# Optimization experiments

Measured on AMD Instinct MI355X. Metric: run time of the kernel, lower is better.

The kernel has to match this reference:

```python
import jax, jax.numpy as jnp
import numpy as np

FEAT, NHID, NHALF, NCLS = 256, 512, 256, 2

def _xavier(key, shape):
    fan_in, fan_out = shape[0], shape[1]
    limit = np.sqrt(6.0 / (fan_in + fan_out))
    return jax.random.uniform(key, shape, jnp.float32, -limit, limit)

def setup_inputs() -> dict:
    key = jax.random.key(0)
    ks = jax.random.split(key, 10)
    B, N = 64, 1024
    x = jax.random.normal(ks[0], (B, N, FEAT), jnp.float32)
    adj = jax.random.uniform(ks[1], (B, N, N), jnp.float32)
    adj = adj / jnp.sum(adj, axis=-1, keepdims=True)  # row-normalized (mean aggregation)
    return {
        "x": x, "adj": adj,
        "W1": _xavier(ks[2], (2 * FEAT, NHID)), "b1": jnp.zeros((NHID,), jnp.float32),
        "W2": _xavier(ks[3], (2 * NHID, NHID)), "b2": jnp.zeros((NHID,), jnp.float32),
        "W3": _xavier(ks[4], (2 * NHID, NHALF)), "b3": jnp.zeros((NHALF,), jnp.float32),
        "W4": _xavier(ks[5], (2 * NHALF, NHALF)), "b4": jnp.zeros((NHALF,), jnp.float32),
        "Wc1": _xavier(ks[6], (NHALF, NHALF)), "bc1": jnp.zeros((NHALF,), jnp.float32),
        "alpha": jnp.full((NHALF,), 0.25, jnp.float32),  # PReLU per-channel slope
        "Wc2": _xavier(ks[7], (NHALF, NCLS)), "bc2": jnp.zeros((NCLS,), jnp.float32),
    }

def _gconv(x, adj, W, b):
    # MeanAggregator: bmm(adj, x); GraphConv: relu(cat([x, agg]) @ W + b)
    agg = jnp.einsum('bnm,bmd->bnd', adj, x)
    cat = jnp.concatenate([x, agg], axis=-1)
    return jax.nn.relu(jnp.einsum('bnd,df->bnf', cat, W) + b)

def reference(x, adj, W1, b1, W2, b2, W3, b3, W4, b4, Wc1, bc1, alpha, Wc2, bc2):
    h = _gconv(x, adj, W1, b1)
    h = _gconv(h, adj, W2, b2)
    h = _gconv(h, adj, W3, b3)
    h = _gconv(h, adj, W4, b4)
    h = h.reshape(-1, h.shape[-1])  # [B*N, nhid_half]
    h = h @ Wc1 + bc1
    h = jnp.where(h > 0, h, alpha * h)  # PReLU
    logits = h @ Wc2 + bc2
    return jax.nn.log_softmax(logits, axis=-1)
```

## Files before the change

### kernel.cpp

```cpp
#include <hip/hip_runtime.h>
#include <hip/hip_bf16.h>
#include <cmath>

typedef _Float16 f16;
typedef __attribute__((ext_vector_type(4))) _Float16 f16x4;
typedef __attribute__((ext_vector_type(8))) _Float16 f16x8;
typedef __attribute__((ext_vector_type(4))) float f32x4;

__device__ inline void gload_lds16(const f16* g, f16* l) {
  __builtin_amdgcn_global_load_lds(
      (const __attribute__((address_space(1))) unsigned int*)g,
      (__attribute__((address_space(3))) unsigned int*)l, 16, 0, 0);
}

__global__ __launch_bounds__(256) void cvt_f32_f16(const float* __restrict__ in,
                                                   f16* __restrict__ out, long n) {
  long stride = (long)gridDim.x * 256 * 8;
  for (long i = ((long)blockIdx.x * 256 + threadIdx.x) * 8; i < n; i += stride) {
    float4 a = *(const float4*)(in + i);
    float4 b = *(const float4*)(in + i + 4);
    f16x8 o;
    o[0] = (f16)a.x; o[1] = (f16)a.y; o[2] = (f16)a.z; o[3] = (f16)a.w;
    o[4] = (f16)b.x; o[5] = (f16)b.y; o[6] = (f16)b.z; o[7] = (f16)b.w;
    *(f16x8*)(out + i) = o;
  }
}

__global__ __launch_bounds__(256) void transpose_cvt(const float* __restrict__ in,
                                                     f16* __restrict__ out,
                                                     int R, int C, long sIn, long sOut) {
  in  += (long)blockIdx.z * sIn;
  out += (long)blockIdx.z * sOut;
  __shared__ f16 t[32][34];
  const int tx = threadIdx.x, ty = threadIdx.y;
  const int c0 = blockIdx.x * 32, r0 = blockIdx.y * 32;
  #pragma unroll
  for (int j = 0; j < 32; j += 8)
    t[ty + j][tx] = (f16)in[(long)(r0 + ty + j) * C + (c0 + tx)];
  __syncthreads();
  #pragma unroll
  for (int j = 0; j < 32; j += 8)
    out[(long)(c0 + ty + j) * R + (r0 + tx)] = t[tx][ty + j];
}

template <int ACT, bool DUAL, bool WRITE_T>
__global__ __launch_bounds__(256) void gemm_nt(
    const f16* __restrict__ A1, int lda1,
    const f16* __restrict__ B1, int ldb1, int K1,
    const f16* __restrict__ A2, int lda2,
    const f16* __restrict__ B2, int ldb2, int K2,
    const float* __restrict__ bias, const float* __restrict__ alpha,
    f16* __restrict__ C, int ldc, f16* __restrict__ CT,
    long sA, long sB, long sC) {
  __shared__ f16 As[128 * 32];
  __shared__ f16 Bs[128 * 32];
  const int tid = threadIdx.x;
  const int z = blockIdx.z;
  const f16* pA1 = A1 + (long)z * sA;
  const f16* pB1 = B1 + (long)z * sB;
  f16* pC = C + (long)z * sC;
  const int m0 = blockIdx.x * 128, n0 = blockIdx.y * 128;
  const int lane = tid & 63, wid = tid >> 6;
  const int wm = (wid >> 1) * 64, wn = (wid & 1) * 64;
  const int lrow = lane & 15, kg = lane >> 4;

  f32x4 acc[4][4] = {};

  const f16* Ap = pA1;
  const f16* Bp = pB1;
  int ldA = lda1, ldB = ldb1, K = K1;
  for (int phase = 0; phase < (DUAL ? 2 : 1); ++phase) {
    if (DUAL && phase == 1) { Ap = A2; Bp = B2; ldA = lda2; ldB = ldb2; K = K2; }
    for (int k0 = 0; k0 < K; k0 += 32) {
      const f16* baseA = Ap + (long)m0 * ldA + k0;
      const f16* baseB = Bp + (long)n0 * ldB + k0;
      f16* dA = As + (tid & 192) * 8;
      f16* dB = Bs + (tid & 192) * 8;
      gload_lds16(baseA + (tid >> 2) * ldA + (tid & 3) * 8, dA);
      gload_lds16(baseB + (tid >> 2) * ldB + (tid & 3) * 8, dB);
      {
        const int idx = 256 + tid;
        gload_lds16(baseA + (idx >> 2) * ldA + (idx & 3) * 8, dA + 2048);
        gload_lds16(baseB + (idx >> 2) * ldB + (idx & 3) * 8, dB + 2048);
      }
      __syncthreads();
      f16x8 af[4], bf[4];
      #pragma unroll
      for (int m = 0; m < 4; ++m)
        af[m] = *(const f16x8*)&As[(wm + m * 16 + lrow) * 32 + kg * 8];
      #pragma unroll
      for (int n = 0; n < 4; ++n)
        bf[n] = *(const f16x8*)&Bs[(wn + n * 16 + lrow) * 32 + kg * 8];
      #pragma unroll
      for (int m = 0; m < 4; ++m)
        #pragma unroll
        for (int n = 0; n < 4; ++n)
          acc[m][n] = __builtin_amdgcn_mfma_f32_16x16x32_f16(af[m], bf[n], acc[m][n], 0, 0, 0);
      __syncthreads();
    }
  }

  #pragma unroll
  for (int n = 0; n < 4; ++n) {
    const int gn = n0 + wn + n * 16 + lrow;
    const float bv = bias ? bias[gn] : 0.0f;
    const float av = (ACT == 2) ? alpha[gn] : 0.0f;
    #pragma unroll
    for (int m = 0; m < 4; ++m) {
      const int rg0 = m0 + wm + m * 16 + kg * 4;
      f16 tv[4];
      #pragma unroll
      for (int r = 0; r < 4; ++r) {
        float v = acc[m][n][r] + bv;
        if (ACT == 1) v = fmaxf(v, 0.0f);
        if (ACT == 2) v = (v > 0.0f) ? v : av * v;
        const f16 h = (f16)v;
        tv[r] = h;
        pC[(long)(rg0 + r) * ldc + gn] = h;
      }
      if (WRITE_T) {
        const int b = rg0 >> 10, node = rg0 & 1023;
        f16x4 pk;
        pk[0] = tv[0]; pk[1] = tv[1]; pk[2] = tv[2]; pk[3] = tv[3];
        *(f16x4*)&CT[((long)b * ldc + gn) * 1024 + node] = pk;
      }
    }
  }
}

__global__ __launch_bounds__(256) void logits_lsm(const f16* __restrict__ hc,
                                                  const float* __restrict__ Wc2,
                                                  const float* __restrict__ bc2,
                                                  float* __restrict__ out) {
  __shared__ float w[512];
  __shared__ float bb[2];
  const int t = threadIdx.x;
  w[t] = Wc2[t];
  w[t + 256] = Wc2[t + 256];
  if (t < 2) bb[t] = bc2[t];
  __syncthreads();
  const long row = (long)blockIdx.x * 256 + t;
  const f16* hr = hc + row * 256;
  float l0 = 0.f, l1 = 0.f;
  #pragma unroll 4
  for (int d0 = 0; d0 < 256; d0 += 8) {
    f16x8 v = *(const f16x8*)(hr + d0);
    #pragma unroll
    for (int j = 0; j < 8; ++j) {
      const float p = (float)v[j];
      l0 += p * w[(d0 + j) * 2];
      l1 += p * w[(d0 + j) * 2 + 1];
    }
  }
  l0 += bb[0];
  l1 += bb[1];
  const float mx = fmaxf(l0, l1);
  const float lse = mx + logf(expf(l0 - mx) + expf(l1 - mx));
  out[row * 2] = l0 - lse;
  out[row * 2 + 1] = l1 - lse;
}

extern "C" void kernel_launch(void* const* d_in, const int* in_sizes, int n_in,
                              void* d_out, int out_size, void* d_ws, size_t ws_size,
                              hipStream_t stream) {
  const float* x     = (const float*)d_in[0];
  const float* adj   = (const float*)d_in[1];
  const float* W1    = (const float*)d_in[2];
  const float* b1    = (const float*)d_in[3];
  const float* W2    = (const float*)d_in[4];
  const float* b2    = (const float*)d_in[5];
  const float* W3    = (const float*)d_in[6];
  const float* b3    = (const float*)d_in[7];
  const float* W4    = (const float*)d_in[8];
  const float* b4    = (const float*)d_in[9];
  const float* Wc1   = (const float*)d_in[10];
  const float* bc1   = (const float*)d_in[11];
  const float* alpha = (const float*)d_in[12];
  const float* Wc2   = (const float*)d_in[13];
  const float* bc2   = (const float*)d_in[14];
  float* out = (float*)d_out;

  char* ws = (char*)d_ws;
  f16* adjB = (f16*)(ws + 0L);
  f16* xN   = (f16*)(ws + 134217728L);
  f16* xT   = (f16*)(ws + 167772160L);
  f16* agg  = (f16*)(ws + 201326592L);
  f16* hAN  = (f16*)(ws + 268435456L);
  f16* hAT  = (f16*)(ws + 335544320L);
  f16* hBN  = (f16*)(ws + 402653184L);
  f16* hBT  = (f16*)(ws + 469762048L);
  f16* WT1  = (f16*)(ws + 536870912L);
  f16* WT2  = (f16*)(ws + 537395200L);
  f16* WT3  = (f16*)(ws + 538443776L);
  f16* WT4  = (f16*)(ws + 538968064L);
  f16* WTc1 = (f16*)(ws + 539230208L);
  if (ws_size < (size_t)539361280L) return;

  const dim3 tb(32, 8, 1);

  cvt_f32_f16<<<2048, 256, 0, stream>>>(adj, adjB, 64L * 1024 * 1024);
  cvt_f32_f16<<<1024, 256, 0, stream>>>(x, xN, 64L * 1024 * 256);
  transpose_cvt<<<dim3(8, 32, 64), tb, 0, stream>>>(x, xT, 1024, 256, 1024L * 256, 256L * 1024);
  transpose_cvt<<<dim3(16, 16, 1), tb, 0, stream>>>(W1, WT1, 512, 512, 0, 0);
  transpose_cvt<<<dim3(16, 32, 1), tb, 0, stream>>>(W2, WT2, 1024, 512, 0, 0);
  transpose_cvt<<<dim3(8, 32, 1), tb, 0, stream>>>(W3, WT3, 1024, 256, 0, 0);
  transpose_cvt<<<dim3(8, 16, 1), tb, 0, stream>>>(W4, WT4, 512, 256, 0, 0);
  transpose_cvt<<<dim3(8, 8, 1), tb, 0, stream>>>(Wc1, WTc1, 256, 256, 0, 0);

  gemm_nt<0, false, false><<<dim3(8, 2, 64), 256, 0, stream>>>(
      adjB, 1024, xT, 1024, 1024,
      nullptr, 0, nullptr, 0, 0,
      nullptr, nullptr, agg, 256, nullptr,
      1024L * 1024, 256L * 1024, 1024L * 256);
  gemm_nt<1, true, true><<<dim3(512, 4, 1), 256, 0, stream>>>(
      xN, 256, WT1, 512, 256,
      agg, 256, WT1 + 256, 512, 256,
      b1, nullptr, hAN, 512, hAT, 0, 0, 0);

  gemm_nt<0, false, false><<<dim3(8, 4, 64), 256, 0, stream>>>(
      adjB, 1024, hAT, 1024, 1024,
      nullptr, 0, nullptr, 0, 0,
      nullptr, nullptr, agg, 512, nullptr,
      1024L * 1024, 512L * 1024, 1024L * 512);
  gemm_nt<1, true, true><<<dim3(512, 4, 1), 256, 0, stream>>>(
      hAN, 512, WT2, 1024, 512,
      agg, 512, WT2 + 512, 1024, 512,
      b2, nullptr, hBN, 512, hBT, 0, 0, 0);

  gemm_nt<0, false, false><<<dim3(8, 4, 64), 256, 0, stream>>>(
      adjB, 1024, hBT, 1024, 1024,
      nullptr, 0, nullptr, 0, 0,
      nullptr, nullptr, agg, 512, nullptr,
      1024L * 1024, 512L * 1024, 1024L * 512);
  gemm_nt<1, true, true><<<dim3(512, 2, 1), 256, 0, stream>>>(
      hBN, 512, WT3, 1024, 512,
      agg, 512, WT3 + 512, 1024, 512,
      b3, nullptr, hAN, 256, hAT, 0, 0, 0);

  gemm_nt<0, false, false><<<dim3(8, 2, 64), 256, 0, stream>>>(
      adjB, 1024, hAT, 1024, 1024,
      nullptr, 0, nullptr, 0, 0,
      nullptr, nullptr, agg, 256, nullptr,
      1024L * 1024, 256L * 1024, 1024L * 256);
  gemm_nt<1, true, false><<<dim3(512, 2, 1), 256, 0, stream>>>(
      hAN, 256, WT4, 512, 256,
      agg, 256, WT4 + 256, 512, 256,
      b4, nullptr, hBN, 256, nullptr, 0, 0, 0);

  gemm_nt<2, false, false><<<dim3(512, 2, 1), 256, 0, stream>>>(
      hBN, 256, WTc1, 256, 256,
      nullptr, 0, nullptr, 0, 0,
      bc1, alpha, hAN, 256, nullptr, 0, 0, 0);

  logits_lsm<<<256, 256, 0, stream>>>(hAN, Wc2, bc2, out);
}
```

Before: 1.276 ms.

## Replace 128x128 GEMM with double-buffered 256x256 tile, swizzled LDS and split-K-step MFMA

The GEMM kernel moves from 128x128 tiles with BK=32 and a single LDS buffer to 256x256 tiles with BK=64 and 512 threads. Global-to-LDS loads are double-buffered and prefetched two steps ahead, with explicit vmcnt waits and barriers in place of full syncthreads. LDS columns are XOR-swizzled to avoid bank conflicts, and s_setprio is raised around the MFMA bursts. This should raise arithmetic intensity and hide load latency, at the cost of 128KB of LDS per block, higher register pressure and fewer blocks for the small batched GEMMs.

Measured after the change: 1.125 ms. -11.8%, faster.

```diff
diff --git a/kernel.cpp b/kernel.cpp
--- a/kernel.cpp
+++ b/kernel.cpp
@@ -44,70 +44,105 @@
 }
 
 template <int ACT, bool DUAL, bool WRITE_T>
-__global__ __launch_bounds__(256) void gemm_nt(
+__global__ __launch_bounds__(512, 2) void gemm256(
     const f16* __restrict__ A1, int lda1,
-    const f16* __restrict__ B1, int ldb1, int K1,
+    const f16* __restrict__ B1, int ldb1, int k1,
     const f16* __restrict__ A2, int lda2,
-    const f16* __restrict__ B2, int ldb2, int K2,
+    const f16* __restrict__ B2, int ldb2, int k2,
     const float* __restrict__ bias, const float* __restrict__ alpha,
     f16* __restrict__ C, int ldc, f16* __restrict__ CT,
     long sA, long sB, long sC) {
-  __shared__ f16 As[128 * 32];
-  __shared__ f16 Bs[128 * 32];
+  __shared__ f16 As[2][16384];
+  __shared__ f16 Bs[2][16384];
   const int tid = threadIdx.x;
   const int z = blockIdx.z;
-  const f16* pA1 = A1 + (long)z * sA;
-  const f16* pB1 = B1 + (long)z * sB;
+  const f16* a1 = A1 + (long)z * sA;
+  const f16* b1 = B1 + (long)z * sB;
   f16* pC = C + (long)z * sC;
-  const int m0 = blockIdx.x * 128, n0 = blockIdx.y * 128;
-  const int lane = tid & 63, wid = tid >> 6;
-  const int wm = (wid >> 1) * 64, wn = (wid & 1) * 64;
+  const int m0 = blockIdx.x * 256, n0 = blockIdx.y * 256;
+  const int lane = tid & 63, w = tid >> 6;
+  const int wr = w >> 2, wc = w & 3;
   const int lrow = lane & 15, kg = lane >> 4;
-
-  f32x4 acc[4][4] = {};
-
-  const f16* Ap = pA1;
-  const f16* Bp = pB1;
-  int ldA = lda1, ldB = ldb1, K = K1;
-  for (int phase = 0; phase < (DUAL ? 2 : 1); ++phase) {
-    if (DUAL && phase == 1) { Ap = A2; Bp = B2; ldA = lda2; ldB = ldb2; K = K2; }
-    for (int k0 = 0; k0 < K; k0 += 32) {
-      const f16* baseA = Ap + (long)m0 * ldA + k0;
-      const f16* baseB = Bp + (long)n0 * ldB + k0;
-      f16* dA = As + (tid & 192) * 8;
-      f16* dB = Bs + (tid & 192) * 8;
-      gload_lds16(baseA + (tid >> 2) * ldA + (tid & 3) * 8, dA);
-      gload_lds16(baseB + (tid >> 2) * ldB + (tid & 3) * 8, dB);
-      {
-        const int idx = 256 + tid;
-        gload_lds16(baseA + (idx >> 2) * ldA + (idx & 3) * 8, dA + 2048);
-        gload_lds16(baseB + (idx >> 2) * ldB + (idx & 3) * 8, dB + 2048);
-      }
-      __syncthreads();
-      f16x8 af[4], bf[4];
-      #pragma unroll
-      for (int m = 0; m < 4; ++m)
-        af[m] = *(const f16x8*)&As[(wm + m * 16 + lrow) * 32 + kg * 8];
+  const int NT1 = k1 >> 6;
+  const int NT = NT1 + (DUAL ? (k2 >> 6) : 0);
+
+  const int srow = tid >> 3;
+  const int cg = (tid & 7) ^ (srow & 7);
+  const int ldst = (tid & 448) * 8;
+
+  const int swz = lrow & 7;
+  const int ac0 = ((0 * 4 + kg) ^ swz) * 8;
+  const int ac1 = ((4 + kg) ^ swz) * 8;
+  const int arow = wr * 128 + lrow;
+  const int brow = wc * 64 + lrow;
+
+  f32x4 acc[8][4] = {};
+
+  auto stage = [&](int kt) {
+    const f16 *Ab, *Bb; int la, lb, kk;
+    if (!DUAL || kt < NT1) { Ab = a1; Bb = b1; la = lda1; lb = ldb1; kk = kt << 6; }
+    else { Ab = A2; Bb = B2; la = lda2; lb = ldb2; kk = (kt - NT1) << 6; }
+    const int bs = kt & 1;
+    #pragma unroll
+    for (int j = 0; j < 4; ++j)
+      gload_lds16(Ab + (long)(m0 + srow + j * 64) * la + kk + cg * 8,
+                  &As[bs][j * 4096 + ldst]);
+    #pragma unroll
+    for (int j = 0; j < 4; ++j)
+      gload_lds16(Bb + (long)(n0 + srow + j * 64) * lb + kk + cg * 8,
+                  &Bs[bs][j * 4096 + ldst]);
+  };
+
+  stage(0);
+  stage(1);
+  asm volatile("s_waitcnt vmcnt(8)\n\ts_barrier" ::: "memory");
+
+  for (int t = 0; t < NT; ++t) {
+    const int bs = t & 1;
+    f16x8 af[8], bf[4];
+    #pragma unroll
+    for (int m = 0; m < 8; ++m)
+      af[m] = *(const f16x8*)&As[bs][(arow + m * 16) * 64 + ac0];
+    #pragma unroll
+    for (int n = 0; n < 4; ++n)
+      bf[n] = *(const f16x8*)&Bs[bs][(brow + n * 16) * 64 + ac0];
+    __builtin_amdgcn_s_setprio(1);
+    #pragma unroll
+    for (int m = 0; m < 8; ++m)
       #pragma unroll
       for (int n = 0; n < 4; ++n)
-        bf[n] = *(const f16x8*)&Bs[(wn + n * 16 + lrow) * 32 + kg * 8];
+        acc[m][n] = __builtin_amdgcn_mfma_f32_16x16x32_f16(af[m], bf[n], acc[m][n], 0, 0, 0);
+    __builtin_amdgcn_s_setprio(0);
+    f16x8 ag[8], bg[4];
+    #pragma unroll
+    for (int m = 0; m < 8; ++m)
+      ag[m] = *(const f16x8*)&As[bs][(arow + m * 16) * 64 + ac1];
+    #pragma unroll
+    for (int n = 0; n < 4; ++n)
+      bg[n] = *(const f16x8*)&Bs[bs][(brow + n * 16) * 64 + ac1];
+    asm volatile("s_waitcnt lgkmcnt(0)\n\ts_barrier" ::: "memory");
+    if (t + 2 < NT) stage(t + 2);
+    __builtin_amdgcn_s_setprio(1);
+    #pragma unroll
+    for (int m = 0; m < 8; ++m)
       #pragma unroll
-      for (int m = 0; m < 4; ++m)
-        #pragma unroll
-        for (int n = 0; n < 4; ++n)
-          acc[m][n] = __builtin_amdgcn_mfma_f32_16x16x32_f16(af[m], bf[n], acc[m][n], 0, 0, 0);
-      __syncthreads();
-    }
+      for (int n = 0; n < 4; ++n)
+        acc[m][n] = __builtin_amdgcn_mfma_f32_16x16x32_f16(ag[m], bg[n], acc[m][n], 0, 0, 0);
+    __builtin_amdgcn_s_setprio(0);
+    if (t + 2 < NT)
+      asm volatile("s_waitcnt vmcnt(8)\n\ts_barrier" ::: "memory");
+    else if (t + 1 < NT)
+      asm volatile("s_waitcnt vmcnt(0)\n\ts_barrier" ::: "memory");
   }
 
   #pragma unroll
   for (int n = 0; n < 4; ++n) {
-    const int gn = n0 + wn + n * 16 + lrow;
+    const int gn = n0 + wc * 64 + n * 16 + lrow;
     const float bv = bias ? bias[gn] : 0.0f;
     const float av = (ACT == 2) ? alpha[gn] : 0.0f;
     #pragma unroll
-    for (int m = 0; m < 4; ++m) {
-      const int rg0 = m0 + wm + m * 16 + kg * 4;
+    for (int m = 0; m < 8; ++m) {
+      const int rg0 = m0 + wr * 128 + m * 16 + kg * 4;
       f16 tv[4];
       #pragma unroll
       for (int r = 0; r < 4; ++r) {
@@ -207,47 +242,47 @@
   transpose_cvt<<<dim3(8, 16, 1), tb, 0, stream>>>(W4, WT4, 512, 256, 0, 0);
   transpose_cvt<<<dim3(8, 8, 1), tb, 0, stream>>>(Wc1, WTc1, 256, 256, 0, 0);
 
-  gemm_nt<0, false, false><<<dim3(8, 2, 64), 256, 0, stream>>>(
+  gemm256<0, false, false><<<dim3(4, 1, 64), 512, 0, stream>>>(
       adjB, 1024, xT, 1024, 1024,
       nullptr, 0, nullptr, 0, 0,
       nullptr, nullptr, agg, 256, nullptr,
       1024L * 1024, 256L * 1024, 1024L * 256);
-  gemm_nt<1, true, true><<<dim3(512, 4, 1), 256, 0, stream>>>(
+  gemm256<1, true, true><<<dim3(256, 2, 1), 512, 0, stream>>>(
       xN, 256, WT1, 512, 256,
       agg, 256, WT1 + 256, 512, 256,
       b1, nullptr, hAN, 512, hAT, 0, 0, 0);
 
-  gemm_nt<0, false, false><<<dim3(8, 4, 64), 256, 0, stream>>>(
+  gemm256<0, false, false><<<dim3(4, 2, 64), 512, 0, stream>>>(
       adjB, 1024, hAT, 1024, 1024,
       nullptr, 0, nullptr, 0, 0,
       nullptr, nullptr, agg, 512, nullptr,
       1024L * 1024, 512L * 1024, 1024L * 512);
-  gemm_nt<1, true, true><<<dim3(512, 4, 1), 256, 0, stream>>>(
+  gemm256<1, true, true><<<dim3(256, 2, 1), 512, 0, stream>>>(
       hAN, 512, WT2, 1024, 512,
       agg, 512, WT2 + 512, 1024, 512,
       b2, nullptr, hBN, 512, hBT, 0, 0, 0);
 
-  gemm_nt<0, false, false><<<dim3(8, 4, 64), 256, 0, stream>>>(
+  gemm256<0, false, false><<<dim3(4, 2, 64), 512, 0, stream>>>(
       adjB, 1024, hBT, 1024, 1024,
       nullptr, 0, nullptr, 0, 0,
       nullptr, nullptr, agg, 512, nullptr,
       1024L * 1024, 512L * 1024, 1024L * 512);
-  gemm_nt<1, true, true><<<dim3(512, 2, 1), 256, 0, stream>>>(
+  gemm256<1, true, true><<<dim3(256, 1, 1), 512, 0, stream>>>(
       hBN, 512, WT3, 1024, 512,
       agg, 512, WT3 + 512, 1024, 512,
       b3, nullptr, hAN, 256, hAT, 0, 0, 0);
 
-  gemm_nt<0, false, false><<<dim3(8, 2, 64), 256, 0, stream>>>(
+  gemm256<0, false, false><<<dim3(4, 1, 64), 512, 0, stream>>>(
       adjB, 1024, hAT, 1024, 1024,
       nullptr, 0, nullptr, 0, 0,
       nullptr, nullptr, agg, 256, nullptr,
       1024L * 1024, 256L * 1024, 1024L * 256);
-  gemm_nt<1, true, false><<<dim3(512, 2, 1), 256, 0, stream>>>(
+  gemm256<1, true, false><<<dim3(256, 1, 1), 512, 0, stream>>>(
       hAN, 256, WT4, 512, 256,
       agg, 256, WT4 + 256, 512, 256,
       b4, nullptr, hBN, 256, nullptr, 0, 0, 0);
 
-  gemm_nt<2, false, false><<<dim3(512, 2, 1), 256, 0, stream>>>(
+  gemm256<2, false, false><<<dim3(256, 1, 1), 512, 0, stream>>>(
       hBN, 256, WTc1, 256, 256,
       nullptr, 0, nullptr, 0, 0,
       bc1, alpha, hAN, 256, nullptr, 0, 0, 0);
```

## Double-buffer GEMM LDS tiles with swizzle, XCD-aware block remap, fuse prep kernels

Applied to the files above, without the earlier changes.

The GEMM kernel now double-buffers its A/B LDS tiles, so the next K-tile's global-to-LDS loads overlap the MFMA work on the current tile, using explicit vmcnt waits and one barrier per step. LDS columns are XOR-swizzled to cut bank conflicts, and s_setprio raises priority around the MFMA block. A 1D grid is remapped so consecutive blocks spread across the 8 XCDs, with launch bounds requesting 3 blocks per CU. Separate cast/transpose launches for x and the five weights are folded into two prep kernels, which doubles LDS use and depends on the hand-written wait counts being correct.

New measurement: 1.085 ms. -15.0%, faster.

```diff
diff --git a/kernel.cpp b/kernel.cpp
--- a/kernel.cpp
+++ b/kernel.cpp
@@ -26,15 +26,48 @@
   }
 }
 
-__global__ __launch_bounds__(256) void transpose_cvt(const float* __restrict__ in,
-                                                     f16* __restrict__ out,
-                                                     int R, int C, long sIn, long sOut) {
-  in  += (long)blockIdx.z * sIn;
-  out += (long)blockIdx.z * sOut;
+__global__ __launch_bounds__(256) void xprep(const float* __restrict__ in,
+                                             f16* __restrict__ outN,
+                                             f16* __restrict__ outT,
+                                             int R, int C, long sIn) {
+  in   += (long)blockIdx.z * sIn;
+  outN += (long)blockIdx.z * sIn;
+  outT += (long)blockIdx.z * sIn;
   __shared__ f16 t[32][34];
   const int tx = threadIdx.x, ty = threadIdx.y;
   const int c0 = blockIdx.x * 32, r0 = blockIdx.y * 32;
   #pragma unroll
+  for (int j = 0; j < 32; j += 8) {
+    const f16 v = (f16)in[(long)(r0 + ty + j) * C + (c0 + tx)];
+    t[ty + j][tx] = v;
+    outN[(long)(r0 + ty + j) * C + (c0 + tx)] = v;
+  }
+  __syncthreads();
+  #pragma unroll
+  for (int j = 0; j < 32; j += 8)
+    outT[(long)(c0 + ty + j) * R + (r0 + tx)] = t[tx][ty + j];
+}
+
+__global__ __launch_bounds__(256) void wprep(const float* __restrict__ W1,
+                                             const float* __restrict__ W2,
+                                             const float* __restrict__ W3,
+                                             const float* __restrict__ W4,
+                                             const float* __restrict__ Wc1,
+                                             f16* __restrict__ T1, f16* __restrict__ T2,
+                                             f16* __restrict__ T3, f16* __restrict__ T4,
+                                             f16* __restrict__ Tc1) {
+  int b = blockIdx.x;
+  const float* in; f16* out; int R, C;
+  if (b < 256)       {          in = W1;  out = T1;  R = 512;  C = 512; }
+  else if (b < 768)  { b -= 256;  in = W2;  out = T2;  R = 1024; C = 512; }
+  else if (b < 1024) { b -= 768;  in = W3;  out = T3;  R = 1024; C = 256; }
+  else if (b < 1152) { b -= 1024; in = W4;  out = T4;  R = 512;  C = 256; }
+  else               { b -= 1152; in = Wc1; out = Tc1; R = 256;  C = 256; }
+  const int nbx = C >> 5;
+  const int c0 = (b % nbx) * 32, r0 = (b / nbx) * 32;
+  __shared__ f16 t[32][34];
+  const int tx = threadIdx.x & 31, ty = threadIdx.x >> 5;
+  #pragma unroll
   for (int j = 0; j < 32; j += 8)
     t[ty + j][tx] = (f16)in[(long)(r0 + ty + j) * C + (c0 + tx)];
   __syncthreads();
@@ -44,70 +77,96 @@
 }
 
 template <int ACT, bool DUAL, bool WRITE_T>
-__global__ __launch_bounds__(256) void gemm_nt(
+__global__ __launch_bounds__(256, 3) void gemm128(
     const f16* __restrict__ A1, int lda1,
-    const f16* __restrict__ B1, int ldb1, int K1,
+    const f16* __restrict__ B1, int ldb1, int k1,
     const f16* __restrict__ A2, int lda2,
-    const f16* __restrict__ B2, int ldb2, int K2,
+    const f16* __restrict__ B2, int ldb2, int k2,
     const float* __restrict__ bias, const float* __restrict__ alpha,
     f16* __restrict__ C, int ldc, f16* __restrict__ CT,
-    long sA, long sB, long sC) {
-  __shared__ f16 As[128 * 32];
-  __shared__ f16 Bs[128 * 32];
+    long sA, long sB, long sC, int gxs, int gys, int nwg) {
+  __shared__ __align__(16) f16 As[2][4096];
+  __shared__ __align__(16) f16 Bs[2][4096];
+  const int wg = blockIdx.x;
+  const int lid = (wg & 7) * (nwg >> 3) + (wg >> 3);
+  const int by = lid & ((1 << gys) - 1);
+  const int bx = (lid >> gys) & ((1 << gxs) - 1);
+  const int z = lid >> (gxs + gys);
+
   const int tid = threadIdx.x;
-  const int z = blockIdx.z;
-  const f16* pA1 = A1 + (long)z * sA;
-  const f16* pB1 = B1 + (long)z * sB;
+  const f16* a1 = A1 + (long)z * sA;
+  const f16* b1 = B1 + (long)z * sB;
   f16* pC = C + (long)z * sC;
-  const int m0 = blockIdx.x * 128, n0 = blockIdx.y * 128;
-  const int lane = tid & 63, wid = tid >> 6;
-  const int wm = (wid >> 1) * 64, wn = (wid & 1) * 64;
+  const int m0 = bx * 128, n0 = by * 128;
+  const int lane = tid & 63, w = tid >> 6;
+  const int wr = w >> 1, wc = w & 1;
   const int lrow = lane & 15, kg = lane >> 4;
+  const int NT1 = k1 >> 5;
+  const int NT = NT1 + (DUAL ? (k2 >> 5) : 0);
+
+  const int srow = tid >> 2;
+  const int cg = (tid & 3) ^ ((srow >> 1) & 3);
+  const int ldst = (tid & 192) * 8;
+
+  const int swz = (lrow >> 1) & 3;
+  const int ac = (kg ^ swz) * 8;
+  const int arow = wr * 64 + lrow;
+  const int brow = wc * 64 + lrow;
 
   f32x4 acc[4][4] = {};
 
-  const f16* Ap = pA1;
-  const f16* Bp = pB1;
-  int ldA = lda1, ldB = ldb1, K = K1;
-  for (int phase = 0; phase < (DUAL ? 2 : 1); ++phase) {
-    if (DUAL && phase == 1) { Ap = A2; Bp = B2; ldA = lda2; ldB = ldb2; K = K2; }
-    for (int k0 = 0; k0 < K; k0 += 32) {
-      const f16* baseA = Ap + (long)m0 * ldA + k0;
-      const f16* baseB = Bp + (long)n0 * ldB + k0;
-      f16* dA = As + (tid & 192) * 8;
-      f16* dB = Bs + (tid & 192) * 8;
-      gload_lds16(baseA + (tid >> 2) * ldA + (tid & 3) * 8, dA);
-      gload_lds16(baseB + (tid >> 2) * ldB + (tid & 3) * 8, dB);
-      {
-        const int idx = 256 + tid;
-        gload_lds16(baseA + (idx >> 2) * ldA + (idx & 3) * 8, dA + 2048);
-        gload_lds16(baseB + (idx >> 2) * ldB + (idx & 3) * 8, dB + 2048);
-      }
-      __syncthreads();
-      f16x8 af[4], bf[4];
-      #pragma unroll
-      for (int m = 0; m < 4; ++m)
-        af[m] = *(const f16x8*)&As[(wm + m * 16 + lrow) * 32 + kg * 8];
+  auto stage = [&](int kt, int buf) {
+    const f16 *Ab, *Bb; int la, lb, kk;
+    if (!DUAL || kt < NT1) { Ab = a1; Bb = b1; la = lda1; lb = ldb1; kk = kt << 5; }
+    else { Ab = A2; Bb = B2; la = lda2; lb = ldb2; kk = (kt - NT1) << 5; }
+    #pragma unroll
+    for (int j = 0; j < 2; ++j)
+      gload_lds16(Ab + (long)(m0 + srow + j * 64) * la + kk + cg * 8,
+                  &As[buf][j * 2048 + ldst]);
+    #pragma unroll
+    for (int j = 0; j < 2; ++j)
+      gload_lds16(Bb + (long)(n0 + srow + j * 64) * lb + kk + cg * 8,
+                  &Bs[buf][j * 2048 + ldst]);
+  };
+
+  stage(0, 0);
+  int buf = 0;
+  for (int t = 0; t < NT; ++t) {
+    if (t + 1 < NT) {
+      stage(t + 1, buf ^ 1);
+      asm volatile("s_waitcnt vmcnt(4)" ::: "memory");
+    } else {
+      asm volatile("s_waitcnt vmcnt(0)" ::: "memory");
+    }
+    __builtin_amdgcn_s_barrier();
+    f16x8 af[4], bf[4];
+    #pragma unroll
+    for (int m = 0; m < 4; ++m)
+      af[m] = *(const f16x8*)&As[buf][(arow + m * 16) * 32 + ac];
+    #pragma unroll
+    for (int n = 0; n < 4; ++n)
+      bf[n] = *(const f16x8*)&Bs[buf][(brow + n * 16) * 32 + ac];
+    asm volatile("s_waitcnt lgkmcnt(0)" ::: "memory");
+    __builtin_amdgcn_sched_barrier(0);
+    __builtin_amdgcn_s_setprio(1);
+    #pragma unroll
+    for (int m = 0; m < 4; ++m)
       #pragma unroll
       for (int n = 0; n < 4; ++n)
-        bf[n] = *(const f16x8*)&Bs[(wn + n * 16 + lrow) * 32 + kg * 8];
-      #pragma unroll
-      for (int m = 0; m < 4; ++m)
-        #pragma unroll
-        for (int n = 0; n < 4; ++n)
-          acc[m][n] = __builtin_amdgcn_mfma_f32_16x16x32_f16(af[m], bf[n], acc[m][n], 0, 0, 0);
-      __syncthreads();
-    }
+        acc[m][n] = __builtin_amdgcn_mfma_f32_16x16x32_f16(af[m], bf[n], acc[m][n], 0, 0, 0);
+    __builtin_amdgcn_s_setprio(0);
+    if (t + 1 < NT) __builtin_amdgcn_s_barrier();
+    buf ^= 1;
   }
 
   #pragma unroll
   for (int n = 0; n < 4; ++n) {
-    const int gn = n0 + wn + n * 16 + lrow;
+    const int gn = n0 + wc * 64 + n * 16 + lrow;
     const float bv = bias ? bias[gn] : 0.0f;
     const float av = (ACT == 2) ? alpha[gn] : 0.0f;
     #pragma unroll
     for (int m = 0; m < 4; ++m) {
-      const int rg0 = m0 + wm + m * 16 + kg * 4;
+      const int rg0 = m0 + wr * 64 + m * 16 + kg * 4;
       f16 tv[4];
       #pragma unroll
       for (int r = 0; r < 4; ++r) {
@@ -196,61 +255,54 @@
   f16* WTc1 = (f16*)(ws + 539230208L);
   if (ws_size < (size_t)539361280L) return;
 
-  const dim3 tb(32, 8, 1);
-
   cvt_f32_f16<<<2048, 256, 0, stream>>>(adj, adjB, 64L * 1024 * 1024);
-  cvt_f32_f16<<<1024, 256, 0, stream>>>(x, xN, 64L * 1024 * 256);
-  transpose_cvt<<<dim3(8, 32, 64), tb, 0, stream>>>(x, xT, 1024, 256, 1024L * 256, 256L * 1024);
-  transpose_cvt<<<dim3(16, 16, 1), tb, 0, stream>>>(W1, WT1, 512, 512, 0, 0);
-  transpose_cvt<<<dim3(16, 32, 1), tb, 0, stream>>>(W2, WT2, 1024, 512, 0, 0);
-  transpose_cvt<<<dim3(8, 32, 1), tb, 0, stream>>>(W3, WT3, 1024, 256, 0, 0);
-  transpose_cvt<<<dim3(8, 16, 1), tb, 0, stream>>>(W4, WT4, 512, 256, 0, 0);
-  transpose_cvt<<<dim3(8, 8, 1), tb, 0, stream>>>(Wc1, WTc1, 256, 256, 0, 0);
-
-  gemm_nt<0, false, false><<<dim3(8, 2, 64), 256, 0, stream>>>(
+  xprep<<<dim3(8, 32, 64), dim3(32, 8, 1), 0, stream>>>(x, xN, xT, 1024, 256, 1024L * 256);
+  wprep<<<1216, 256, 0, stream>>>(W1, W2, W3, W4, Wc1, WT1, WT2, WT3, WT4, WTc1);
+
+  gemm128<0, false, false><<<1024, 256, 0, stream>>>(
       adjB, 1024, xT, 1024, 1024,
       nullptr, 0, nullptr, 0, 0,
       nullptr, nullptr, agg, 256, nullptr,
-      1024L * 1024, 256L * 1024, 1024L * 256);
-  gemm_nt<1, true, true><<<dim3(512, 4, 1), 256, 0, stream>>>(
+      1024L * 1024, 256L * 1024, 1024L * 256, 3, 1, 1024);
+  gemm128<1, true, true><<<2048, 256, 0, stream>>>(
       xN, 256, WT1, 512, 256,
       agg, 256, WT1 + 256, 512, 256,
-      b1, nullptr, hAN, 512, hAT, 0, 0, 0);
-
-  gemm_nt<0, false, false><<<dim3(8, 4, 64), 256, 0, stream>>>(
+      b1, nullptr, hAN, 512, hAT, 0, 0, 0, 9, 2, 2048);
+
+  gemm128<0, false, false><<<2048, 256, 0, stream>>>(
       adjB, 1024, hAT, 1024, 1024,
       nullptr, 0, nullptr, 0, 0,
       nullptr, nullptr, agg, 512, nullptr,
-      1024L * 1024, 512L * 1024, 1024L * 512);
-  gemm_nt<1, true, true><<<dim3(512, 4, 1), 256, 0, stream>>>(
+      1024L * 1024, 512L * 1024, 1024L * 512, 3, 2, 2048);
+  gemm128<1, true, true><<<2048, 256, 0, stream>>>(
       hAN, 512, WT2, 1024, 512,
       agg, 512, WT2 + 512, 1024, 512,
-      b2, nullptr, hBN, 512, hBT, 0, 0, 0);
-
-  gemm_nt<0, false, false><<<dim3(8, 4, 64), 256, 0, stream>>>(
+      b2, nullptr, hBN, 512, hBT, 0, 0, 0, 9, 2, 2048);
+
+  gemm128<0, false, false><<<2048, 256, 0, stream>>>(
       adjB, 1024, hBT, 1024, 1024,
       nullptr, 0, nullptr, 0, 0,
       nullptr, nullptr, agg, 512, nullptr,
-      1024L * 1024, 512L * 1024, 1024L * 512);
-  gemm_nt<1, true, true><<<dim3(512, 2, 1), 256, 0, stream>>>(
+      1024L * 1024, 512L * 1024, 1024L * 512, 3, 2, 2048);
+  gemm128<1, true, true><<<1024, 256, 0, stream>>>(
       hBN, 512, WT3, 1024, 512,
       agg, 512, WT3 + 512, 1024, 512,
-      b3, nullptr, hAN, 256, hAT, 0, 0, 0);
-
-  gemm_nt<0, false, false><<<dim3(8, 2, 64), 256, 0, stream>>>(
+      b3, nullptr, hAN, 256, hAT, 0, 0, 0, 9, 1, 1024);
+
+  gemm128<0, false, false><<<1024, 256, 0, stream>>>(
       adjB, 1024, hAT, 1024, 1024,
       nullptr, 0, nullptr, 0, 0,
       nullptr, nullptr, agg, 256, nullptr,
-      1024L * 1024, 256L * 1024, 1024L * 256);
-  gemm_nt<1, true, false><<<dim3(512, 2, 1), 256, 0, stream>>>(
+      1024L * 1024, 256L * 1024, 1024L * 256, 3, 1, 1024);
+  gemm128<1, true, false><<<1024, 256, 0, stream>>>(
       hAN, 256, WT4, 512, 256,
       agg, 256, WT4 + 256, 512, 256,
-      b4, nullptr, hBN, 256, nullptr, 0, 0, 0);
-
-  gemm_nt<2, false, false><<<dim3(512, 2, 1), 256, 0, stream>>>(
+      b4, nullptr, hBN, 256, nullptr, 0, 0, 0, 9, 1, 1024);
+
+  gemm128<2, false, false><<<1024, 256, 0, stream>>>(
       hBN, 256, WTc1, 256, 256,
       nullptr, 0, nullptr, 0, 0,
-      bc1, alpha, hAN, 256, nullptr, 0, 0, 0);
+      bc1, alpha, hAN, 256, nullptr, 0, 0, 0, 9, 1, 1024);
 
   logits_lsm<<<256, 256, 0, stream>>>(hAN, Wc2, bc2, out);
 }
```
